# Kernel optimization log

Hardware: AMD Instinct MI355X
Metric: run time of the kernel (lower is better)

The kernel has to match this reference:

```python
import jax, jax.numpy as jnp
import numpy as np

N = 100000      # nodes
E = 1600000     # edges
D_IN = 16       # input_dim
D_H = 32        # hidden_dim
D_OUT = 1       # output_dim
N_ITERS = 2
D_CAT = D_H + D_IN          # node feature after cat([H, X])
D_EDGE = 2 * D_CAT          # edge MLP input dim


def setup_inputs() -> dict:
    key = jax.random.key(0)
    ks = jax.random.split(key, 10)
    x = jax.random.normal(ks[0], (N, D_IN), jnp.float32)
    edge_index = jax.random.randint(ks[1], (2, E), 0, N, dtype=jnp.int32)
    # inputnet: Linear(D_IN -> D_H) + Tanh
    W_in = jax.random.normal(ks[2], (D_H, D_IN), jnp.float32) / np.sqrt(D_IN)
    b_in = jnp.zeros((D_H,), jnp.float32)
    # convnn (EdgeConv nn): Linear(D_EDGE -> D_H) + Sigmoid
    W_c = jax.random.normal(ks[3], (D_H, D_EDGE), jnp.float32) / np.sqrt(D_EDGE)
    b_c = jnp.zeros((D_H,), jnp.float32)
    # outputnet: Linear(D_H -> D_OUT) + Sigmoid
    W_out = jax.random.normal(ks[4], (D_OUT, D_H), jnp.float32) / np.sqrt(D_H)
    b_out = jnp.zeros((D_OUT,), jnp.float32)
    return {"x": x, "edge_index": edge_index, "W_in": W_in, "b_in": b_in,
            "W_c": W_c, "b_c": b_c, "W_out": W_out, "b_out": b_out}


def reference(x, edge_index, W_in, b_in, W_c, b_c, W_out, b_out):
    src = edge_index[0]  # x_j (source / neighbor)
    dst = edge_index[1]  # x_i (target, aggregation index)

    H = jnp.tanh(x @ W_in.T + b_in)            # [N, D_H]
    feats = jnp.concatenate([H, x], axis=-1)    # [N, D_CAT]

    for _ in range(N_ITERS):
        xi = feats[dst]                          # [E, D_CAT] gather targets
        xj = feats[src]                          # [E, D_CAT] gather sources
        # PyG EdgeConv message: nn(cat([x_i, x_j - x_i]))
        msg = jax.nn.sigmoid(
            jnp.concatenate([xi, xj - xi], axis=-1) @ W_c.T + b_c)  # [E, D_H]
        H = jax.ops.segment_sum(msg, dst, num_segments=N)           # aggr='add'
        feats = jnp.concatenate([H, x], axis=-1)

    sum_H = jnp.mean(H, axis=0)                  # [D_H]
    return jax.nn.sigmoid(sum_H @ W_out.T + b_out)  # [D_OUT]
```

## Files before the change

kernel.cpp:

```cpp
#include <hip/hip_runtime.h>

#define D_H 32
#define NREP 32
#define SLOTS 48
#define BIN_SHIFT 8
#define MAXNB 512
#define BIN_CAP 5120
#define SB 256

__global__ void k_ab0(const float* __restrict__ x, const float* __restrict__ W_in,
                      const float* __restrict__ b_in, const float* __restrict__ W_c,
                      const float* __restrict__ b_c, float* __restrict__ A,
                      float* __restrict__ B, int N) {
    int n = blockIdx.x * blockDim.x + threadIdx.x;
    if (n >= N) return;
    float f[48];
    const float4* xr = (const float4*)(x + (size_t)n * 16);
#pragma unroll
    for (int q = 0; q < 4; ++q) {
        float4 v = xr[q];
        f[32 + 4 * q] = v.x; f[33 + 4 * q] = v.y;
        f[34 + 4 * q] = v.z; f[35 + 4 * q] = v.w;
    }
#pragma unroll
    for (int j = 0; j < 32; ++j) {
        const float* w = W_in + j * 16;
        float acc = b_in[j];
#pragma unroll
        for (int i = 0; i < 16; ++i) acc += f[32 + i] * w[i];
        f[j] = tanhf(acc);
    }
#pragma unroll 4
    for (int j = 0; j < 32; ++j) {
        const float* w = W_c + j * 96;
        float p = b_c[j];
        float bb = 0.f;
#pragma unroll
        for (int i = 0; i < 48; ++i) {
            p  += f[i] * w[i];
            bb += f[i] * w[48 + i];
        }
        A[(size_t)n * D_H + j] = p - bb;
        B[(size_t)n * D_H + j] = bb;
    }
}

__global__ void k_ab1(const float* __restrict__ H, const float* __restrict__ x,
                      const float* __restrict__ W_c, const float* __restrict__ b_c,
                      float* __restrict__ A, float* __restrict__ B, int N) {
    int n = blockIdx.x * blockDim.x + threadIdx.x;
    if (n >= N) return;
    float f[48];
    const float4* hr = (const float4*)(H + (size_t)n * D_H);
#pragma unroll
    for (int q = 0; q < 8; ++q) {
        float4 v = hr[q];
        f[4 * q]     = v.x; f[4 * q + 1] = v.y;
        f[4 * q + 2] = v.z; f[4 * q + 3] = v.w;
    }
    const float4* xr = (const float4*)(x + (size_t)n * 16);
#pragma unroll
    for (int q = 0; q < 4; ++q) {
        float4 v = xr[q];
        f[32 + 4 * q] = v.x; f[33 + 4 * q] = v.y;
        f[34 + 4 * q] = v.z; f[35 + 4 * q] = v.w;
    }
#pragma unroll 4
    for (int j = 0; j < 32; ++j) {
        const float* w = W_c + j * 96;
        float p = b_c[j];
        float bb = 0.f;
#pragma unroll
        for (int i = 0; i < 48; ++i) {
            p  += f[i] * w[i];
            bb += f[i] * w[48 + i];
        }
        A[(size_t)n * D_H + j] = p - bb;
        B[(size_t)n * D_H + j] = bb;
    }
}

__global__ __launch_bounds__(256) void k_bin(const int* __restrict__ src,
                                             const int* __restrict__ dst,
                                             int* __restrict__ binCnt,
                                             unsigned int* __restrict__ ebuf, int E) {
    __shared__ int hist[MAXNB];
    int tid = threadIdx.x;
    int nb = (int)gridDim.y;
    (void)nb;
    for (int i = tid; i < MAXNB; i += 256) hist[i] = 0;
    __syncthreads();
    int chunk = (E + SB - 1) / SB;
    int lo = blockIdx.x * chunk;
    int hi = lo + chunk; if (hi > E) hi = E;
    for (int e = lo + tid; e < hi; e += 256) {
        int b = dst[e] >> BIN_SHIFT;
        atomicAdd(&hist[b], 1);
    }
    __syncthreads();
    for (int b = tid; b < MAXNB; b += 256) {
        int c = hist[b];
        int base = c ? atomicAdd(&binCnt[b], c) : 0;
        hist[b] = b * BIN_CAP + base;
    }
    __syncthreads();
    for (int e = lo + tid; e < hi; e += 256) {
        int d = dst[e];
        int s = src[e];
        int b = d >> BIN_SHIFT;
        int pos = atomicAdd(&hist[b], 1);
        if ((unsigned)(pos - b * BIN_CAP) < (unsigned)BIN_CAP)
            ebuf[pos] = ((unsigned)(d & 255) << 24) | (unsigned)s;
    }
}

__global__ __launch_bounds__(256) void k_place(const int* __restrict__ binCnt,
                                               const unsigned int* __restrict__ ebuf,
                                               int* __restrict__ ssrcp,
                                               int* __restrict__ cntG, int N) {
    __shared__ int cnt[256];
    int tid = threadIdx.x;
    int w = blockIdx.x;
    cnt[tid] = 0;
    __syncthreads();
    int n = binCnt[w]; if (n > BIN_CAP) n = BIN_CAP;
    int base = w * BIN_CAP;
    for (int j = tid; j < n; j += 256) {
        unsigned int v = ebuf[base + j];
        int ld = v >> 24;
        int s = v & 0xFFFFFF;
        int slot = atomicAdd(&cnt[ld], 1);
        if (slot < SLOTS)
            ssrcp[(size_t)((w << BIN_SHIFT) + ld) * SLOTS + slot] = s;
    }
    __syncthreads();
    int node = (w << BIN_SHIFT) + tid;
    if (node < N) cntG[node] = cnt[tid] < SLOTS ? cnt[tid] : SLOTS;
}


__global__ void k_gather1(const int* __restrict__ cntG, const int* __restrict__ ssrcp,
                          const float* __restrict__ A, const float* __restrict__ B,
                          float* __restrict__ H, int N) {
    int t = blockIdx.x * blockDim.x + threadIdx.x;
    int d = t >> 5;
    if (d >= N) return;
    int l = t & 31;
    int q = l & 7;
    int s = l >> 3;
    int len = cntG[d];
    const int* base = ssrcp + (size_t)d * SLOTS;
    float4 a4 = ((const float4*)(A + (size_t)d * D_H))[q];
    float4 acc = {0.f, 0.f, 0.f, 0.f};
    int j = s;
    for (; j + 4 < len; j += 8) {
        int s0 = base[j], s1 = base[j + 4];
        float4 b0 = ((const float4*)(B + (size_t)s0 * D_H))[q];
        float4 b1 = ((const float4*)(B + (size_t)s1 * D_H))[q];
        acc.x += 1.f / (1.f + __expf(-(a4.x + b0.x)));
        acc.y += 1.f / (1.f + __expf(-(a4.y + b0.y)));
        acc.z += 1.f / (1.f + __expf(-(a4.z + b0.z)));
        acc.w += 1.f / (1.f + __expf(-(a4.w + b0.w)));
        acc.x += 1.f / (1.f + __expf(-(a4.x + b1.x)));
        acc.y += 1.f / (1.f + __expf(-(a4.y + b1.y)));
        acc.z += 1.f / (1.f + __expf(-(a4.z + b1.z)));
        acc.w += 1.f / (1.f + __expf(-(a4.w + b1.w)));
    }
    if (j < len) {
        int s0 = base[j];
        float4 b0 = ((const float4*)(B + (size_t)s0 * D_H))[q];
        acc.x += 1.f / (1.f + __expf(-(a4.x + b0.x)));
        acc.y += 1.f / (1.f + __expf(-(a4.y + b0.y)));
        acc.z += 1.f / (1.f + __expf(-(a4.z + b0.z)));
        acc.w += 1.f / (1.f + __expf(-(a4.w + b0.w)));
    }
    acc.x += __shfl_xor(acc.x, 8);  acc.y += __shfl_xor(acc.y, 8);
    acc.z += __shfl_xor(acc.z, 8);  acc.w += __shfl_xor(acc.w, 8);
    acc.x += __shfl_xor(acc.x, 16); acc.y += __shfl_xor(acc.y, 16);
    acc.z += __shfl_xor(acc.z, 16); acc.w += __shfl_xor(acc.w, 16);
    if (s == 0) ((float4*)(H + (size_t)d * D_H))[q] = acc;
}

__global__ void k_gather2(const int* __restrict__ cntG, const int* __restrict__ ssrcp,
                          const float* __restrict__ A, const float* __restrict__ B,
                          float* __restrict__ Srep, int N) {
    int l = threadIdx.x & 31;
    int slot = threadIdx.x >> 5;
    int q = l & 7;
    int s = l >> 3;
    int d = blockIdx.x * 8 + slot;
    float4 acc = {0.f, 0.f, 0.f, 0.f};
    if (d < N) {
        int len = cntG[d];
        const int* base = ssrcp + (size_t)d * SLOTS;
        float4 a4 = ((const float4*)(A + (size_t)d * D_H))[q];
        int j = s;
        for (; j + 4 < len; j += 8) {
            int s0 = base[j], s1 = base[j + 4];
            float4 b0 = ((const float4*)(B + (size_t)s0 * D_H))[q];
            float4 b1 = ((const float4*)(B + (size_t)s1 * D_H))[q];
            acc.x += 1.f / (1.f + __expf(-(a4.x + b0.x)));
            acc.y += 1.f / (1.f + __expf(-(a4.y + b0.y)));
            acc.z += 1.f / (1.f + __expf(-(a4.z + b0.z)));
            acc.w += 1.f / (1.f + __expf(-(a4.w + b0.w)));
            acc.x += 1.f / (1.f + __expf(-(a4.x + b1.x)));
            acc.y += 1.f / (1.f + __expf(-(a4.y + b1.y)));
            acc.z += 1.f / (1.f + __expf(-(a4.z + b1.z)));
            acc.w += 1.f / (1.f + __expf(-(a4.w + b1.w)));
        }
        if (j < len) {
            int s0 = base[j];
            float4 b0 = ((const float4*)(B + (size_t)s0 * D_H))[q];
            acc.x += 1.f / (1.f + __expf(-(a4.x + b0.x)));
            acc.y += 1.f / (1.f + __expf(-(a4.y + b0.y)));
            acc.z += 1.f / (1.f + __expf(-(a4.z + b0.z)));
            acc.w += 1.f / (1.f + __expf(-(a4.w + b0.w)));
        }
    }
    acc.x += __shfl_xor(acc.x, 8);  acc.y += __shfl_xor(acc.y, 8);
    acc.z += __shfl_xor(acc.z, 8);  acc.w += __shfl_xor(acc.w, 8);
    acc.x += __shfl_xor(acc.x, 16); acc.y += __shfl_xor(acc.y, 16);
    acc.z += __shfl_xor(acc.z, 16); acc.w += __shfl_xor(acc.w, 16);
    __shared__ float red[8][32];
    if (s == 0) {
        red[slot][4 * q + 0] = acc.x;
        red[slot][4 * q + 1] = acc.y;
        red[slot][4 * q + 2] = acc.z;
        red[slot][4 * q + 3] = acc.w;
    }
    __syncthreads();
    if (threadIdx.x < 32) {
        float sm = 0.f;
#pragma unroll
        for (int r = 0; r < 8; ++r) sm += red[r][threadIdx.x];
        unsafeAtomicAdd(&Srep[(blockIdx.x & (NREP - 1)) * D_H + threadIdx.x], sm);
    }
}

__global__ void k_final(const float* __restrict__ Srep, const float* __restrict__ W_out,
                        const float* __restrict__ b_out, float* __restrict__ out,
                        float invN) {
    int j = threadIdx.x;
    float v = 0.f;
    if (j < 32) {
        float s = 0.f;
#pragma unroll
        for (int r = 0; r < NREP; ++r) s += Srep[r * D_H + j];
        v = s * invN * W_out[j];
    }
#pragma unroll
    for (int off = 32; off > 0; off >>= 1) v += __shfl_down(v, off);
    if (j == 0) out[0] = 1.f / (1.f + __expf(-(v + b_out[0])));
}

extern "C" void kernel_launch(void* const* d_in, const int* in_sizes, int n_in,
                              void* d_out, int out_size, void* d_ws, size_t ws_size,
                              hipStream_t stream) {
    const float* x     = (const float*)d_in[0];
    const int*   ei    = (const int*)d_in[1];
    const float* W_in  = (const float*)d_in[2];
    const float* b_in  = (const float*)d_in[3];
    const float* W_c   = (const float*)d_in[4];
    const float* b_c   = (const float*)d_in[5];
    const float* W_out = (const float*)d_in[6];
    const float* b_out = (const float*)d_in[7];

    const int N = in_sizes[0] / 16;
    const int E = in_sizes[1] / 2;
    const int* src = ei;
    const int* dst = ei + E;

    const int NB = (N + 255) >> BIN_SHIFT;

    float* H    = (float*)d_ws;
    float* A    = H + (size_t)N * D_H;
    float* B    = A + (size_t)N * D_H;
    float* Srep = B + (size_t)N * D_H;
    int*   cntG   = (int*)(Srep + NREP * D_H);
    int*   binCnt = cntG + N;
    int*   ssrcp  = binCnt + MAXNB;
    unsigned int* ebuf = (unsigned int*)A;

    float* out = (float*)d_out;

    hipMemsetAsync(binCnt, 0, MAXNB * sizeof(int), stream);
    k_bin<<<SB, 256, 0, stream>>>(src, dst, binCnt, ebuf, E);
    k_place<<<NB, 256, 0, stream>>>(binCnt, ebuf, ssrcp, cntG, N);

    k_ab0<<<(N + 255) / 256, 256, 0, stream>>>(x, W_in, b_in, W_c, b_c, A, B, N);
    k_gather1<<<(int)(((size_t)N * 32 + 255) / 256), 256, 0, stream>>>(cntG, ssrcp, A, B, H, N);

    k_ab1<<<(N + 255) / 256, 256, 0, stream>>>(H, x, W_c, b_c, A, B, N);
    hipMemsetAsync(Srep, 0, NREP * D_H * sizeof(float), stream);
    k_gather2<<<(N + 7) / 8, 256, 0, stream>>>(cntG, ssrcp, A, B, Srep, N);

    k_final<<<1, 64, 0, stream>>>(Srep, W_out, b_out, out, 1.f / (float)N);
}
```

Measured before the change: 289.4 us.

## Stage node features in shared memory and split outputs across thread groups

The per-node A/B projection kernels now process 64 nodes per 256-thread block. Input rows are loaded coalesced into a transposed shared-memory tile, each of four thread groups computes 8 of the 32 output channels, and results are staged back through shared memory for coalesced float4 stores. Previously each thread handled one node and did strided 128-byte row reads and per-element writes. The change also aims for more parallelism per node, at the cost of extra barriers and shared-memory traffic. The bin buffer alias moves from A to H so it does not overlap the new layout.

```diff
diff --git a/kernel.cpp b/kernel.cpp
--- a/kernel.cpp
+++ b/kernel.cpp
@@ -7,31 +7,20 @@
 #define MAXNB 512
 #define BIN_CAP 5120
 #define SB 256
-
-__global__ void k_ab0(const float* __restrict__ x, const float* __restrict__ W_in,
-                      const float* __restrict__ b_in, const float* __restrict__ W_c,
-                      const float* __restrict__ b_c, float* __restrict__ A,
-                      float* __restrict__ B, int N) {
-    int n = blockIdx.x * blockDim.x + threadIdx.x;
-    if (n >= N) return;
+#define NPB 64
+
+
+__device__ __forceinline__ void conv_and_flush(
+        float st[48][NPB + 1], const float* __restrict__ W_c,
+        const float* __restrict__ b_c, float* __restrict__ A, float* __restrict__ B,
+        int N, int n0, int tid, int nl, int qq) {
     float f[48];
-    const float4* xr = (const float4*)(x + (size_t)n * 16);
-#pragma unroll
-    for (int q = 0; q < 4; ++q) {
-        float4 v = xr[q];
-        f[32 + 4 * q] = v.x; f[33 + 4 * q] = v.y;
-        f[34 + 4 * q] = v.z; f[35 + 4 * q] = v.w;
-    }
-#pragma unroll
-    for (int j = 0; j < 32; ++j) {
-        const float* w = W_in + j * 16;
-        float acc = b_in[j];
-#pragma unroll
-        for (int i = 0; i < 16; ++i) acc += f[32 + i] * w[i];
-        f[j] = tanhf(acc);
-    }
-#pragma unroll 4
-    for (int j = 0; j < 32; ++j) {
+#pragma unroll
+    for (int i = 0; i < 48; ++i) f[i] = st[i][nl];
+    float pr[8], br[8];
+#pragma unroll 2
+    for (int jj = 0; jj < 8; ++jj) {
+        int j = qq * 8 + jj;
         const float* w = W_c + j * 96;
         float p = b_c[j];
         float bb = 0.f;
@@ -40,44 +29,109 @@
             p  += f[i] * w[i];
             bb += f[i] * w[48 + i];
         }
-        A[(size_t)n * D_H + j] = p - bb;
-        B[(size_t)n * D_H + j] = bb;
-    }
-}
-
-__global__ void k_ab1(const float* __restrict__ H, const float* __restrict__ x,
+        pr[jj] = p - bb;
+        br[jj] = bb;
+    }
+    __syncthreads();
+#pragma unroll
+    for (int jj = 0; jj < 8; ++jj) st[qq * 8 + jj][nl] = pr[jj];
+    __syncthreads();
+    float4* A4 = (float4*)(A + (size_t)n0 * D_H);
+#pragma unroll
+    for (int k = 0; k < 2; ++k) {
+        int i4 = k * 256 + tid;
+        int nn = i4 >> 3;
+        int j0 = (i4 & 7) * 4;
+        if (n0 + nn < N) {
+            float4 v = {st[j0][nn], st[j0 + 1][nn], st[j0 + 2][nn], st[j0 + 3][nn]};
+            A4[i4] = v;
+        }
+    }
+    __syncthreads();
+#pragma unroll
+    for (int jj = 0; jj < 8; ++jj) st[qq * 8 + jj][nl] = br[jj];
+    __syncthreads();
+    float4* B4 = (float4*)(B + (size_t)n0 * D_H);
+#pragma unroll
+    for (int k = 0; k < 2; ++k) {
+        int i4 = k * 256 + tid;
+        int nn = i4 >> 3;
+        int j0 = (i4 & 7) * 4;
+        if (n0 + nn < N) {
+            float4 v = {st[j0][nn], st[j0 + 1][nn], st[j0 + 2][nn], st[j0 + 3][nn]};
+            B4[i4] = v;
+        }
+    }
+}
+
+__global__ __launch_bounds__(256) void k_ab0(const float* __restrict__ x,
+                      const float* __restrict__ W_in, const float* __restrict__ b_in,
                       const float* __restrict__ W_c, const float* __restrict__ b_c,
                       float* __restrict__ A, float* __restrict__ B, int N) {
-    int n = blockIdx.x * blockDim.x + threadIdx.x;
-    if (n >= N) return;
-    float f[48];
-    const float4* hr = (const float4*)(H + (size_t)n * D_H);
-#pragma unroll
-    for (int q = 0; q < 8; ++q) {
-        float4 v = hr[q];
-        f[4 * q]     = v.x; f[4 * q + 1] = v.y;
-        f[4 * q + 2] = v.z; f[4 * q + 3] = v.w;
-    }
-    const float4* xr = (const float4*)(x + (size_t)n * 16);
-#pragma unroll
-    for (int q = 0; q < 4; ++q) {
-        float4 v = xr[q];
-        f[32 + 4 * q] = v.x; f[33 + 4 * q] = v.y;
-        f[34 + 4 * q] = v.z; f[35 + 4 * q] = v.w;
-    }
-#pragma unroll 4
-    for (int j = 0; j < 32; ++j) {
-        const float* w = W_c + j * 96;
-        float p = b_c[j];
-        float bb = 0.f;
-#pragma unroll
-        for (int i = 0; i < 48; ++i) {
-            p  += f[i] * w[i];
-            bb += f[i] * w[48 + i];
-        }
-        A[(size_t)n * D_H + j] = p - bb;
-        B[(size_t)n * D_H + j] = bb;
-    }
+    __shared__ float st[48][NPB + 1];
+    int tid = threadIdx.x;
+    int n0 = blockIdx.x * NPB;
+    int nl = tid & (NPB - 1);
+    int qq = tid >> 6;
+    {
+        int row = tid >> 2, c = tid & 3;
+        float4 v = {0.f, 0.f, 0.f, 0.f};
+        if (n0 + row < N) v = ((const float4*)(x + (size_t)(n0 + row) * 16))[c];
+        st[32 + 4 * c + 0][row] = v.x;
+        st[32 + 4 * c + 1][row] = v.y;
+        st[32 + 4 * c + 2][row] = v.z;
+        st[32 + 4 * c + 3][row] = v.w;
+    }
+    __syncthreads();
+    {
+        float xf[16];
+#pragma unroll
+        for (int i = 0; i < 16; ++i) xf[i] = st[32 + i][nl];
+#pragma unroll
+        for (int jj = 0; jj < 8; ++jj) {
+            int j = qq * 8 + jj;
+            const float* w = W_in + j * 16;
+            float acc = b_in[j];
+#pragma unroll
+            for (int i = 0; i < 16; ++i) acc += xf[i] * w[i];
+            st[j][nl] = tanhf(acc);
+        }
+    }
+    __syncthreads();
+    conv_and_flush(st, W_c, b_c, A, B, N, n0, tid, nl, qq);
+}
+
+__global__ __launch_bounds__(256) void k_ab1(const float* __restrict__ H,
+                      const float* __restrict__ x, const float* __restrict__ W_c,
+                      const float* __restrict__ b_c, float* __restrict__ A,
+                      float* __restrict__ B, int N) {
+    __shared__ float st[48][NPB + 1];
+    int tid = threadIdx.x;
+    int n0 = blockIdx.x * NPB;
+    int nl = tid & (NPB - 1);
+    int qq = tid >> 6;
+#pragma unroll
+    for (int k = 0; k < 2; ++k) {
+        int i = k * 256 + tid;
+        int row = i >> 3, c = i & 7;
+        float4 v = {0.f, 0.f, 0.f, 0.f};
+        if (n0 + row < N) v = ((const float4*)(H + (size_t)(n0 + row) * D_H))[c];
+        st[4 * c + 0][row] = v.x;
+        st[4 * c + 1][row] = v.y;
+        st[4 * c + 2][row] = v.z;
+        st[4 * c + 3][row] = v.w;
+    }
+    {
+        int row = tid >> 2, c = tid & 3;
+        float4 v = {0.f, 0.f, 0.f, 0.f};
+        if (n0 + row < N) v = ((const float4*)(x + (size_t)(n0 + row) * 16))[c];
+        st[32 + 4 * c + 0][row] = v.x;
+        st[32 + 4 * c + 1][row] = v.y;
+        st[32 + 4 * c + 2][row] = v.z;
+        st[32 + 4 * c + 3][row] = v.w;
+    }
+    __syncthreads();
+    conv_and_flush(st, W_c, b_c, A, B, N, n0, tid, nl, qq);
 }
 
 __global__ __launch_bounds__(256) void k_bin(const int* __restrict__ src,
@@ -86,8 +140,6 @@
                                              unsigned int* __restrict__ ebuf, int E) {
     __shared__ int hist[MAXNB];
     int tid = threadIdx.x;
-    int nb = (int)gridDim.y;
-    (void)nb;
     for (int i = tid; i < MAXNB; i += 256) hist[i] = 0;
     __syncthreads();
     int chunk = (E + SB - 1) / SB;
@@ -279,18 +331,20 @@
     int*   cntG   = (int*)(Srep + NREP * D_H);
     int*   binCnt = cntG + N;
     int*   ssrcp  = binCnt + MAXNB;
-    unsigned int* ebuf = (unsigned int*)A;
+    unsigned int* ebuf = (unsigned int*)H;
 
     float* out = (float*)d_out;
+
+    const int abBlocks = (N + NPB - 1) / NPB;
 
     hipMemsetAsync(binCnt, 0, MAXNB * sizeof(int), stream);
     k_bin<<<SB, 256, 0, stream>>>(src, dst, binCnt, ebuf, E);
     k_place<<<NB, 256, 0, stream>>>(binCnt, ebuf, ssrcp, cntG, N);
 
-    k_ab0<<<(N + 255) / 256, 256, 0, stream>>>(x, W_in, b_in, W_c, b_c, A, B, N);
+    k_ab0<<<abBlocks, 256, 0, stream>>>(x, W_in, b_in, W_c, b_c, A, B, N);
     k_gather1<<<(int)(((size_t)N * 32 + 255) / 256), 256, 0, stream>>>(cntG, ssrcp, A, B, H, N);
 
-    k_ab1<<<(N + 255) / 256, 256, 0, stream>>>(H, x, W_c, b_c, A, B, N);
+    k_ab1<<<abBlocks, 256, 0, stream>>>(H, x, W_c, b_c, A, B, N);
     hipMemsetAsync(Srep, 0, NREP * D_H * sizeof(float), stream);
     k_gather2<<<(N + 7) / 8, 256, 0, stream>>>(cntG, ssrcp, A, B, Srep, N);
 
```

Result: no change. 291.9 us (+0.9%).
